# Performance work log

Hardware: AMD Instinct MI355X
Metric: run time of the kernel (lower is better)

## Reference

```python
import jax, jax.numpy as jnp
import numpy as np

D_MODEL = 2048
N_STATE = 256          # power of two
RANK = 64
LEVELS = int(np.log2(N_STATE))  # 8 butterfly levels
B, S = 4, 4096


def setup_inputs() -> dict:
    key = jax.random.key(0)
    ks = jax.random.split(key, 7)
    u = jax.random.normal(ks[0], (B, S, D_MODEL), dtype=jnp.float32)
    # stacked 2x2 butterfly factors, one per level (orthogonal-ish init)
    A_factors = jax.random.normal(ks[1], (LEVELS, 2, 2), dtype=jnp.float32)
    A_factors = A_factors / jnp.linalg.norm(A_factors, axis=-1, keepdims=True)
    W_b_rank = jax.random.normal(ks[2], (D_MODEL, RANK), dtype=jnp.float32) * (1.0 / np.sqrt(D_MODEL))
    W_b_state = jax.random.normal(ks[3], (RANK, N_STATE), dtype=jnp.float32) * (1.0 / np.sqrt(RANK))
    W_c_rank = jax.random.normal(ks[4], (N_STATE, RANK), dtype=jnp.float32) * (1.0 / np.sqrt(N_STATE))
    W_c_model = jax.random.normal(ks[5], (RANK, D_MODEL), dtype=jnp.float32) * (1.0 / np.sqrt(RANK))
    D_vec = jax.random.normal(ks[6], (D_MODEL,), dtype=jnp.float32) * 0.02
    return {"u": u, "A_factors": A_factors, "W_b_rank": W_b_rank,
            "W_b_state": W_b_state, "W_c_rank": W_c_rank,
            "W_c_model": W_c_model, "D_vec": D_vec}


def _apply_butterfly(state, A_factors):
    # state: [B, S, N]; reshape N into LEVELS axes of size 2 and apply a 2x2
    # factor along each axis (contracting the axis with A's FIRST dim, i.e.
    # x @ A, matching tf.matmul(flattened, factor)).
    b, s, n = state.shape
    x = state.reshape((b, s) + (2,) * LEVELS)
    for lvl in range(LEVELS):
        ax = 2 + lvl
        x = jnp.moveaxis(jnp.tensordot(x, A_factors[lvl], axes=[[ax], [0]]), -1, ax)
    return x.reshape(b, s, n)


def reference(u, A_factors, W_b_rank, W_b_state, W_c_rank, W_c_model, D_vec):
    # B path: low-rank projection to state space
    state = (u @ W_b_rank) @ W_b_state              # [B,S,N]
    # A: butterfly-structured state transform
    state = _apply_butterfly(state, A_factors)      # [B,S,N]
    # C path: low-rank projection back to model dim
    y = (state @ W_c_rank) @ W_c_model              # [B,S,D]
    # D: elementwise feedthrough
    return y + D_vec * u
```

## Files before the change

### kernel.cpp

```cpp
#include <hip/hip_runtime.h>

typedef unsigned short ushort_t;
typedef __attribute__((ext_vector_type(8))) short bf16x8;
typedef __attribute__((ext_vector_type(4))) float f32x4;
typedef __attribute__((ext_vector_type(4))) unsigned short us4;

#define DM 2048
#define RK 64

__device__ __forceinline__ ushort_t f2b(float f) {
    union { float f; unsigned u; } x; x.f = f;
    unsigned r = x.u + 0x7fff + ((x.u >> 16) & 1);
    return (ushort_t)(r >> 16);
}

__global__ void k_p1(const float* __restrict__ Wbs, const float* __restrict__ Af,
                     const float* __restrict__ Wcr, float* __restrict__ Mmid) {
    __shared__ float X[64 * 256];
    const int tid = threadIdx.x;

#pragma unroll
    for (int i = 0; i < 16; ++i) {
        int e = (i * 256 + tid) * 4;
        *(float4*)&X[e] = *(const float4*)&Wbs[e];
    }
    __syncthreads();

#pragma unroll
    for (int l = 0; l < 8; ++l) {
        const int bit = 1 << (7 - l);
        const float a00 = Af[l * 4 + 0], a01 = Af[l * 4 + 1];
        const float a10 = Af[l * 4 + 2], a11 = Af[l * 4 + 3];
#pragma unroll 4
        for (int p = 0; p < 32; ++p) {
            int pid = p * 256 + tid;
            int row = pid >> 7;
            int off = pid & 127;
            int lo = off & (bit - 1);
            int n0 = ((off ^ lo) << 1) | lo;
            int n1 = n0 | bit;
            float x0 = X[row * 256 + n0], x1 = X[row * 256 + n1];
            X[row * 256 + n0] = x0 * a00 + x1 * a10;
            X[row * 256 + n1] = x0 * a01 + x1 * a11;
        }
        __syncthreads();
    }

    int g = blockIdx.x * 256 + tid;
    int r1 = g >> 6, r2 = g & 63;
    float s = 0.f;
#pragma unroll 8
    for (int n = 0; n < 256; ++n) s += X[r1 * 256 + n] * Wcr[n * 64 + r2];
    Mmid[g] = s;
}

__global__ void k_p2(const float* __restrict__ Wbr, const float* __restrict__ Mmid,
                     const float* __restrict__ Wcm,
                     ushort_t* __restrict__ WeffT, ushort_t* __restrict__ WcT) {
    const int b = blockIdx.x, tid = threadIdx.x;
    if (b < 32) {
        __shared__ float LW[64][65];
        __shared__ float LM[64 * 64];
#pragma unroll
        for (int i = 0; i < 4; ++i) {
            int e = (i * 256 + tid) * 4;
            int kk = e >> 6, r = e & 63;
            float4 v = *(const float4*)&Wbr[(size_t)b * 4096 + e];
            LW[kk][r] = v.x; LW[kk][r + 1] = v.y; LW[kk][r + 2] = v.z; LW[kk][r + 3] = v.w;
        }
#pragma unroll
        for (int i = 0; i < 4; ++i) {
            int e = (i * 256 + tid) * 4;
            *(float4*)&LM[e] = *(const float4*)&Mmid[e];
        }
        __syncthreads();

        int kk = tid & 63, n0 = (tid >> 6) * 16;
        float acc[16];
#pragma unroll
        for (int j = 0; j < 16; ++j) acc[j] = 0.f;
        for (int r = 0; r < 64; ++r) {
            float wv = LW[kk][r];
            const float* mrow = &LM[r * 64 + n0];
            float4 m0 = *(const float4*)(mrow);
            float4 m1 = *(const float4*)(mrow + 4);
            float4 m2 = *(const float4*)(mrow + 8);
            float4 m3 = *(const float4*)(mrow + 12);
            acc[0] += wv * m0.x; acc[1] += wv * m0.y; acc[2] += wv * m0.z; acc[3] += wv * m0.w;
            acc[4] += wv * m1.x; acc[5] += wv * m1.y; acc[6] += wv * m1.z; acc[7] += wv * m1.w;
            acc[8] += wv * m2.x; acc[9] += wv * m2.y; acc[10] += wv * m2.z; acc[11] += wv * m2.w;
            acc[12] += wv * m3.x; acc[13] += wv * m3.y; acc[14] += wv * m3.z; acc[15] += wv * m3.w;
        }
#pragma unroll
        for (int j = 0; j < 16; ++j)
            WeffT[(size_t)(n0 + j) * DM + b * 64 + kk] = f2b(acc[j]);
    } else {
        __shared__ float LT[64][65];
        const int n0 = (b - 32) * 64;
#pragma unroll
        for (int i = 0; i < 4; ++i) {
            int e = (i * 256 + tid) * 4;
            int k = e >> 6, nn = e & 63;
            float4 v = *(const float4*)&Wcm[(size_t)k * DM + n0 + nn];
            LT[k][nn] = v.x; LT[k][nn + 1] = v.y; LT[k][nn + 2] = v.z; LT[k][nn + 3] = v.w;
        }
        __syncthreads();
#pragma unroll
        for (int i = 0; i < 4; ++i) {
            int e = (i * 256 + tid) * 4;
            int nn = e >> 6, k = e & 63;
            us4 o;
            o.x = f2b(LT[k][nn]); o.y = f2b(LT[k + 1][nn]);
            o.z = f2b(LT[k + 2][nn]); o.w = f2b(LT[k + 3][nn]);
            *(us4*)&WcT[(size_t)(n0 + nn) * RK + k] = o;
        }
    }
}

__global__ __launch_bounds__(512, 5) void k_main(const float* __restrict__ u,
                                                 const ushort_t* __restrict__ WeffT,
                                                 const ushort_t* __restrict__ WcT,
                                                 const float* __restrict__ Dvec,
                                                 float* __restrict__ out) {
    __shared__ float red[8][64][20];
    __shared__ ushort_t tsh[16 * 72];

    const int tid = threadIdx.x;
    const int w = tid >> 6;
    const int lane = tid & 63;
    const int m16 = lane & 15;
    const int quad = lane >> 4;
    const size_t row0 = (size_t)blockIdx.x * 16;
    const float* ub = u + row0 * DM;

    f32x4 acc0 = {0.f, 0.f, 0.f, 0.f}, acc1 = acc0, acc2 = acc0, acc3 = acc0;
    const float* ap = ub + m16 * DM + w * 256 + quad * 8;
    const ushort_t* bp0 = WeffT + (size_t)m16 * DM + w * 256 + quad * 8;
#pragma unroll 4
    for (int ks = 0; ks < 8; ++ks) {
        const int k0 = ks * 32;
        float4 u0 = *(const float4*)(ap + k0);
        float4 u1 = *(const float4*)(ap + k0 + 4);
        bf16x8 a;
        a[0] = (short)f2b(u0.x); a[1] = (short)f2b(u0.y);
        a[2] = (short)f2b(u0.z); a[3] = (short)f2b(u0.w);
        a[4] = (short)f2b(u1.x); a[5] = (short)f2b(u1.y);
        a[6] = (short)f2b(u1.z); a[7] = (short)f2b(u1.w);
        bf16x8 b0 = *(const bf16x8*)(bp0 + k0);
        bf16x8 b1 = *(const bf16x8*)(bp0 + 16 * DM + k0);
        bf16x8 b2 = *(const bf16x8*)(bp0 + 32 * DM + k0);
        bf16x8 b3 = *(const bf16x8*)(bp0 + 48 * DM + k0);
        acc0 = __builtin_amdgcn_mfma_f32_16x16x32_bf16(a, b0, acc0, 0, 0, 0);
        acc1 = __builtin_amdgcn_mfma_f32_16x16x32_bf16(a, b1, acc1, 0, 0, 0);
        acc2 = __builtin_amdgcn_mfma_f32_16x16x32_bf16(a, b2, acc2, 0, 0, 0);
        acc3 = __builtin_amdgcn_mfma_f32_16x16x32_bf16(a, b3, acc3, 0, 0, 0);
    }
    *(f32x4*)&red[w][ 0 + m16][quad * 4] = acc0;
    *(f32x4*)&red[w][16 + m16][quad * 4] = acc1;
    *(f32x4*)&red[w][32 + m16][quad * 4] = acc2;
    *(f32x4*)&red[w][48 + m16][quad * 4] = acc3;
    __syncthreads();

    {
        const int n = tid >> 3, r2 = (tid & 7) * 2;
        float s0 = 0.f, s1 = 0.f;
#pragma unroll
        for (int ww = 0; ww < 8; ++ww) {
            float2 v = *(const float2*)&red[ww][n][r2];
            s0 += v.x; s1 += v.y;
        }
        tsh[r2 * 72 + n]       = f2b(s0);
        tsh[(r2 + 1) * 72 + n] = f2b(s1);
    }
    __syncthreads();

    bf16x8 ta0 = *(const bf16x8*)&tsh[m16 * 72 + quad * 8];
    bf16x8 ta1 = *(const bf16x8*)&tsh[m16 * 72 + 32 + quad * 8];
    const ushort_t* wcb = WcT + (size_t)(w * 256 + m16) * RK + quad * 8;
    const float* u2 = ub + m16 * DM + w * 256 + quad * 4;
    const float* dp = Dvec + w * 256 + quad * 4;
    float* op = out + (row0 + m16) * DM + w * 256 + quad * 4;
#pragma unroll 2
    for (int nt = 0; nt < 16; ++nt) {
        const ushort_t* bp2 = wcb + nt * 16 * RK;
        bf16x8 wb0 = *(const bf16x8*)(bp2);
        bf16x8 wb1 = *(const bf16x8*)(bp2 + 32);
        f32x4 o = {0.f, 0.f, 0.f, 0.f};
        o = __builtin_amdgcn_mfma_f32_16x16x32_bf16(wb0, ta0, o, 0, 0, 0);
        o = __builtin_amdgcn_mfma_f32_16x16x32_bf16(wb1, ta1, o, 0, 0, 0);
        float4 uv = *(const float4*)(u2 + nt * 16);
        float4 dv = *(const float4*)(dp + nt * 16);
        f32x4 st;
        st.x = o[0] + dv.x * uv.x;
        st.y = o[1] + dv.y * uv.y;
        st.z = o[2] + dv.z * uv.z;
        st.w = o[3] + dv.w * uv.w;
        __builtin_nontemporal_store(st, (f32x4*)(op + nt * 16));
    }
}

extern "C" void kernel_launch(void* const* d_in, const int* in_sizes, int n_in,
                              void* d_out, int out_size, void* d_ws, size_t ws_size,
                              hipStream_t stream) {
    (void)in_sizes; (void)n_in; (void)out_size; (void)ws_size;
    const float* u   = (const float*)d_in[0];
    const float* Af  = (const float*)d_in[1];
    const float* Wbr = (const float*)d_in[2];
    const float* Wbs = (const float*)d_in[3];
    const float* Wcr = (const float*)d_in[4];
    const float* Wcm = (const float*)d_in[5];
    const float* Dv  = (const float*)d_in[6];
    float* out = (float*)d_out;

    char* ws = (char*)d_ws;
    float*    Mmid  = (float*)(ws + 0);
    ushort_t* WeffT = (ushort_t*)(ws + 16384);
    ushort_t* WcT   = (ushort_t*)(ws + 278528);

    k_p1<<<16, 256, 0, stream>>>(Wbs, Af, Wcr, Mmid);
    k_p2<<<64, 256, 0, stream>>>(Wbr, Mmid, Wcm, WeffT, WcT);
    k_main<<<1024, 512, 0, stream>>>(u, WeffT, WcT, Dv, out);
}
```

Measured before the change: 327.2 us.

## Split main kernel into staged-LDS projection and separate output GEMM kernels

The fused main kernel is replaced by two kernels. k_a handles 64 rows per block and stages WeffT tiles into swizzled LDS with global_load_lds, so the weights are reused across rows and the cross-wave K-reduction goes away. It writes the 64-rank intermediate to workspace as bf16. k_b keeps WcT fragments and D in registers across 16 row groups and computes output plus feedthrough. The cost is a second pass that reads u again, an extra launch and an intermediate round trip through global memory, and plain stores replace the nontemporal ones.

```diff
diff --git a/kernel.cpp b/kernel.cpp
--- a/kernel.cpp
+++ b/kernel.cpp
@@ -18,14 +18,12 @@
                      const float* __restrict__ Wcr, float* __restrict__ Mmid) {
     __shared__ float X[64 * 256];
     const int tid = threadIdx.x;
-
 #pragma unroll
     for (int i = 0; i < 16; ++i) {
         int e = (i * 256 + tid) * 4;
         *(float4*)&X[e] = *(const float4*)&Wbs[e];
     }
     __syncthreads();
-
 #pragma unroll
     for (int l = 0; l < 8; ++l) {
         const int bit = 1 << (7 - l);
@@ -45,7 +43,6 @@
         }
         __syncthreads();
     }
-
     int g = blockIdx.x * 256 + tid;
     int r1 = g >> 6, r2 = g & 63;
     float s = 0.f;
@@ -74,7 +71,6 @@
             *(float4*)&LM[e] = *(const float4*)&Mmid[e];
         }
         __syncthreads();
-
         int kk = tid & 63, n0 = (tid >> 6) * 16;
         float acc[16];
 #pragma unroll
@@ -117,85 +113,117 @@
     }
 }
 
-__global__ __launch_bounds__(512, 5) void k_main(const float* __restrict__ u,
-                                                 const ushort_t* __restrict__ WeffT,
-                                                 const ushort_t* __restrict__ WcT,
-                                                 const float* __restrict__ Dvec,
-                                                 float* __restrict__ out) {
-    __shared__ float red[8][64][20];
-    __shared__ ushort_t tsh[16 * 72];
+__global__ __launch_bounds__(256) void k_a(const float* __restrict__ u,
+                                           const ushort_t* __restrict__ WeffT,
+                                           ushort_t* __restrict__ tg) {
+    __shared__ ushort_t Wl[64 * 256];
 
     const int tid = threadIdx.x;
     const int w = tid >> 6;
     const int lane = tid & 63;
     const int m16 = lane & 15;
     const int quad = lane >> 4;
-    const size_t row0 = (size_t)blockIdx.x * 16;
-    const float* ub = u + row0 * DM;
-
-    f32x4 acc0 = {0.f, 0.f, 0.f, 0.f}, acc1 = acc0, acc2 = acc0, acc3 = acc0;
-    const float* ap = ub + m16 * DM + w * 256 + quad * 8;
-    const ushort_t* bp0 = WeffT + (size_t)m16 * DM + w * 256 + quad * 8;
-#pragma unroll 4
-    for (int ks = 0; ks < 8; ++ks) {
-        const int k0 = ks * 32;
-        float4 u0 = *(const float4*)(ap + k0);
-        float4 u1 = *(const float4*)(ap + k0 + 4);
-        bf16x8 a;
-        a[0] = (short)f2b(u0.x); a[1] = (short)f2b(u0.y);
-        a[2] = (short)f2b(u0.z); a[3] = (short)f2b(u0.w);
-        a[4] = (short)f2b(u1.x); a[5] = (short)f2b(u1.y);
-        a[6] = (short)f2b(u1.z); a[7] = (short)f2b(u1.w);
-        bf16x8 b0 = *(const bf16x8*)(bp0 + k0);
-        bf16x8 b1 = *(const bf16x8*)(bp0 + 16 * DM + k0);
-        bf16x8 b2 = *(const bf16x8*)(bp0 + 32 * DM + k0);
-        bf16x8 b3 = *(const bf16x8*)(bp0 + 48 * DM + k0);
-        acc0 = __builtin_amdgcn_mfma_f32_16x16x32_bf16(a, b0, acc0, 0, 0, 0);
-        acc1 = __builtin_amdgcn_mfma_f32_16x16x32_bf16(a, b1, acc1, 0, 0, 0);
-        acc2 = __builtin_amdgcn_mfma_f32_16x16x32_bf16(a, b2, acc2, 0, 0, 0);
-        acc3 = __builtin_amdgcn_mfma_f32_16x16x32_bf16(a, b3, acc3, 0, 0, 0);
-    }
-    *(f32x4*)&red[w][ 0 + m16][quad * 4] = acc0;
-    *(f32x4*)&red[w][16 + m16][quad * 4] = acc1;
-    *(f32x4*)&red[w][32 + m16][quad * 4] = acc2;
-    *(f32x4*)&red[w][48 + m16][quad * 4] = acc3;
+    const size_t r0 = (size_t)blockIdx.x * 64;
+
+    const float* ap = u + (r0 + w * 16 + m16) * DM + quad * 8;
+
+    f32x4 acc[4];
+#pragma unroll
+    for (int j = 0; j < 4; ++j) acc[j] = (f32x4){0.f, 0.f, 0.f, 0.f};
+
+    for (int s = 0; s < 8; ++s) {
+        __syncthreads();
+#pragma unroll
+        for (int j = 0; j < 8; ++j) {
+            int n = (w << 4) + j * 2 + (lane >> 5);
+            int p = lane & 31;
+            int chi = p ^ (n & 7);
+            const ushort_t* gp = WeffT + (size_t)n * DM + s * 256 + chi * 8;
+            __builtin_amdgcn_global_load_lds(
+                (const __attribute__((address_space(1))) void*)gp,
+                (__attribute__((address_space(3))) void*)&Wl[((w << 4) + j * 2) * 256],
+                16, 0, 0);
+        }
+        __syncthreads();
+
+#pragma unroll
+        for (int c = 0; c < 8; ++c) {
+            float4 u0 = *(const float4*)(ap + s * 256 + c * 32);
+            float4 u1 = *(const float4*)(ap + s * 256 + c * 32 + 4);
+            bf16x8 a;
+            a[0] = (short)f2b(u0.x); a[1] = (short)f2b(u0.y);
+            a[2] = (short)f2b(u0.z); a[3] = (short)f2b(u0.w);
+            a[4] = (short)f2b(u1.x); a[5] = (short)f2b(u1.y);
+            a[6] = (short)f2b(u1.z); a[7] = (short)f2b(u1.w);
+#pragma unroll
+            for (int j = 0; j < 4; ++j) {
+                int n = m16 + 16 * j;
+                int chi = ((c << 2) | quad) ^ (n & 7);
+                bf16x8 b = *(const bf16x8*)&Wl[n * 256 + chi * 8];
+                acc[j] = __builtin_amdgcn_mfma_f32_16x16x32_bf16(a, b, acc[j], 0, 0, 0);
+            }
+        }
+    }
+
     __syncthreads();
-
+    ushort_t* tt = Wl;
+#pragma unroll
+    for (int j = 0; j < 4; ++j)
+#pragma unroll
+        for (int i = 0; i < 4; ++i)
+            tt[((w << 4) + quad * 4 + i) * 72 + 16 * j + m16] = f2b(acc[j][i]);
+    __syncthreads();
     {
-        const int n = tid >> 3, r2 = (tid & 7) * 2;
-        float s0 = 0.f, s1 = 0.f;
-#pragma unroll
-        for (int ww = 0; ww < 8; ++ww) {
-            float2 v = *(const float2*)&red[ww][n][r2];
-            s0 += v.x; s1 += v.y;
-        }
-        tsh[r2 * 72 + n]       = f2b(s0);
-        tsh[(r2 + 1) * 72 + n] = f2b(s1);
-    }
-    __syncthreads();
-
-    bf16x8 ta0 = *(const bf16x8*)&tsh[m16 * 72 + quad * 8];
-    bf16x8 ta1 = *(const bf16x8*)&tsh[m16 * 72 + 32 + quad * 8];
-    const ushort_t* wcb = WcT + (size_t)(w * 256 + m16) * RK + quad * 8;
-    const float* u2 = ub + m16 * DM + w * 256 + quad * 4;
-    const float* dp = Dvec + w * 256 + quad * 4;
-    float* op = out + (row0 + m16) * DM + w * 256 + quad * 4;
-#pragma unroll 2
-    for (int nt = 0; nt < 16; ++nt) {
-        const ushort_t* bp2 = wcb + nt * 16 * RK;
-        bf16x8 wb0 = *(const bf16x8*)(bp2);
-        bf16x8 wb1 = *(const bf16x8*)(bp2 + 32);
-        f32x4 o = {0.f, 0.f, 0.f, 0.f};
-        o = __builtin_amdgcn_mfma_f32_16x16x32_bf16(wb0, ta0, o, 0, 0, 0);
-        o = __builtin_amdgcn_mfma_f32_16x16x32_bf16(wb1, ta1, o, 0, 0, 0);
-        float4 uv = *(const float4*)(u2 + nt * 16);
-        float4 dv = *(const float4*)(dp + nt * 16);
-        f32x4 st;
-        st.x = o[0] + dv.x * uv.x;
-        st.y = o[1] + dv.y * uv.y;
-        st.z = o[2] + dv.z * uv.z;
-        st.w = o[3] + dv.w * uv.w;
-        __builtin_nontemporal_store(st, (f32x4*)(op + nt * 16));
+        const int lr = (w << 4) + m16;
+        bf16x8 t0 = *(const bf16x8*)&tt[lr * 72 + quad * 16];
+        bf16x8 t1 = *(const bf16x8*)&tt[lr * 72 + quad * 16 + 8];
+        ushort_t* tp = tg + (r0 + lr) * RK + quad * 16;
+        *(bf16x8*)tp = t0;
+        *(bf16x8*)(tp + 8) = t1;
+    }
+}
+
+__global__ __launch_bounds__(64) void k_b(const ushort_t* __restrict__ tg,
+                                          const float* __restrict__ u,
+                                          const ushort_t* __restrict__ WcT,
+                                          const float* __restrict__ Dvec,
+                                          float* __restrict__ out) {
+    const int lane = threadIdx.x;
+    const int m16 = lane & 15;
+    const int quad = lane >> 4;
+    const size_t r0 = (size_t)(blockIdx.x >> 4) * 256;
+    const int c0 = (blockIdx.x & 15) * 128;
+
+    bf16x8 wb0[8], wb1[8];
+    float4 dvv[8];
+#pragma unroll
+    for (int ct = 0; ct < 8; ++ct) {
+        const ushort_t* p = WcT + (size_t)(c0 + ct * 16 + m16) * RK + quad * 8;
+        wb0[ct] = *(const bf16x8*)(p);
+        wb1[ct] = *(const bf16x8*)(p + 32);
+        dvv[ct] = *(const float4*)(Dvec + c0 + ct * 16 + quad * 4);
+    }
+
+    for (int g = 0; g < 16; ++g) {
+        const size_t rg = r0 + g * 16;
+        const ushort_t* tp = tg + (rg + m16) * RK + quad * 8;
+        bf16x8 ta0 = *(const bf16x8*)(tp);
+        bf16x8 ta1 = *(const bf16x8*)(tp + 32);
+        const float* up = u + (rg + m16) * DM + c0 + quad * 4;
+        float* op = out + (rg + m16) * DM + c0 + quad * 4;
+#pragma unroll
+        for (int ct = 0; ct < 8; ++ct) {
+            f32x4 o = {0.f, 0.f, 0.f, 0.f};
+            o = __builtin_amdgcn_mfma_f32_16x16x32_bf16(wb0[ct], ta0, o, 0, 0, 0);
+            o = __builtin_amdgcn_mfma_f32_16x16x32_bf16(wb1[ct], ta1, o, 0, 0, 0);
+            float4 uv = *(const float4*)(up + ct * 16);
+            f32x4 st;
+            st[0] = o[0] + dvv[ct].x * uv.x;
+            st[1] = o[1] + dvv[ct].y * uv.y;
+            st[2] = o[2] + dvv[ct].z * uv.z;
+            st[3] = o[3] + dvv[ct].w * uv.w;
+            *(f32x4*)(op + ct * 16) = st;
+        }
     }
 }
 
@@ -216,8 +244,10 @@
     float*    Mmid  = (float*)(ws + 0);
     ushort_t* WeffT = (ushort_t*)(ws + 16384);
     ushort_t* WcT   = (ushort_t*)(ws + 278528);
+    ushort_t* tg    = (ushort_t*)(ws + 540672);
 
     k_p1<<<16, 256, 0, stream>>>(Wbs, Af, Wcr, Mmid);
     k_p2<<<64, 256, 0, stream>>>(Wbr, Mmid, Wcm, WeffT, WcT);
-    k_main<<<1024, 512, 0, stream>>>(u, WeffT, WcT, Dv, out);
-}
+    k_a <<<256, 256, 0, stream>>>(u, WeffT, tg);
+    k_b <<<1024, 64, 0, stream>>>(tg, u, WcT, Dv, out);
+}
```

Result: slower. 342.1 us (+4.6%).
